# Performance work log

Measured on AMD Instinct MI355X. Metric: run time of the kernel, lower is better.

## Reference

```python
import jax, jax.numpy as jnp
import numpy as np
import math

B, S, H, NH = 2, 2048, 1024, 16
HD = H // NH


def setup_inputs() -> dict:
    key = jax.random.key(0)
    k1, k2, k3 = jax.random.split(key, 3)
    hidden_states = jax.random.normal(k1, (B, S, H), dtype=jnp.float32)
    attention_mask = jnp.zeros((B, 1, 1, S), dtype=jnp.float32)
    w_qkv = jax.random.normal(k2, (3 * H, H), dtype=jnp.float32) * (1.0 / math.sqrt(H))
    w_out = jax.random.normal(k3, (H, H), dtype=jnp.float32) * (1.0 / math.sqrt(H))
    gate = jnp.ones((NH,), dtype=jnp.float32)
    return {"hidden_states": hidden_states, "attention_mask": attention_mask,
            "w_qkv": w_qkv, "w_out": w_out, "gate": gate}


def reference(hidden_states, attention_mask, w_qkv, w_out, gate):
    b, s, h = hidden_states.shape
    nh, hd = NH, HD
    # fused QKV projection (no bias)
    qkv = hidden_states @ w_qkv.T                      # [b, s, 3h]
    qkv = qkv.reshape(b, s, 3, nh, hd)
    q, k, v = jnp.moveaxis(qkv, 2, 0)                  # each [b, s, nh, hd]
    q = q.transpose(0, 2, 1, 3)                        # [b, nh, s, hd]
    k = k.transpose(0, 2, 1, 3)
    v = v.transpose(0, 2, 1, 3)
    scores = jnp.einsum('bhqd,bhkd->bhqk', q, k) / math.sqrt(hd)
    scores = scores + attention_mask                   # broadcast [b,1,1,s]
    probs = jax.nn.softmax(scores, axis=-1)            # dropout p=0 -> identity
    ctx = jnp.einsum('bhqk,bhkd->bhqd', probs, v)      # [b, nh, s, hd]
    ctx = ctx.transpose(0, 2, 1, 3)                    # [b, s, nh, hd]
    ctx = ctx * gate[None, None, :, None]              # per-head gating
    ctx = ctx.reshape(b, s, h)
    out = ctx @ w_out.T
    # all gates active (> 1e-4) -> active_gates/num_heads == 1, no rescale
    return out
```

## Files before the change

kernel.cpp:

```cpp
#include <hip/hip_runtime.h>
#include <stdint.h>


typedef __attribute__((ext_vector_type(8))) short short8;
typedef __attribute__((ext_vector_type(4))) float floatx4;
typedef __attribute__((ext_vector_type(4))) unsigned int uint4v;
typedef __attribute__((ext_vector_type(2))) unsigned int uint2v;

__device__ __forceinline__ unsigned short f2bf(float f) {
    unsigned int u = __float_as_uint(f);
    unsigned int r = u + 0x7fffu + ((u >> 16) & 1u);
    return (unsigned short)(r >> 16);
}
#if __has_builtin(__builtin_amdgcn_cvt_pk_bf16_f32)
__device__ __forceinline__ unsigned int pack_bf2(float lo, float hi) {
    auto v = __builtin_amdgcn_cvt_pk_bf16_f32(lo, hi);
    return __builtin_bit_cast(unsigned int, v);
}
#else
__device__ __forceinline__ unsigned int pack_bf2(float lo, float hi) {
    unsigned int a = __float_as_uint(lo) + 0x8000u;
    unsigned int b = __float_as_uint(hi) + 0x8000u;
    return __builtin_amdgcn_perm(b, a, 0x07060302u);
}
#endif

#if __has_builtin(__builtin_amdgcn_exp2f)
#define EXP2(x) __builtin_amdgcn_exp2f(x)
#else
#define EXP2(x) exp2f(x)
#endif

__device__ __forceinline__ void gl2lds16(const void* g, void* l) {
    __builtin_amdgcn_global_load_lds(
        (const __attribute__((address_space(1))) unsigned int*)g,
        (__attribute__((address_space(3))) unsigned int*)l, 16, 0, 0);
}

#define MFMA32(a, b, c) __builtin_amdgcn_mfma_f32_16x16x32_bf16((a), (b), (c), 0, 0, 0)

__global__ __launch_bounds__(256)
void cvt_all(const float* __restrict__ a, const float* __restrict__ b,
             const float* __restrict__ c, const float* __restrict__ mask,
             unsigned short* __restrict__ oa, unsigned short* __restrict__ ob,
             unsigned short* __restrict__ oc, float* __restrict__ m2b)
{
    int i = blockIdx.x * 256 + threadIdx.x;
    if (i >= 2097152) {
        int off = i - 2097152;
        float4 v = *(const float4*)(mask + (size_t)off * 4);
        const float L2E = 1.44269504f, C2 = -14.4269504f;
        float4 w;
        w.x = fmaf(v.x, L2E, C2); w.y = fmaf(v.y, L2E, C2);
        w.z = fmaf(v.z, L2E, C2); w.w = fmaf(v.w, L2E, C2);
        *(float4*)(m2b + (size_t)off * 4) = w;
        return;
    }
    const float* src; unsigned short* dst; int off;
    if (i < 1048576)      { src = a; dst = oa; off = i; }
    else if (i < 1835008) { src = b; dst = ob; off = i - 1048576; }
    else                  { src = c; dst = oc; off = i - 1835008; }
    float4 v = *(const float4*)(src + (size_t)off * 4);
    uint2v w;
    w[0] = pack_bf2(v.x, v.y);
    w[1] = pack_bf2(v.z, v.w);
    *(uint2v*)(dst + (size_t)off * 4) = w;
}

template<int MODE, int BN>
__global__ __launch_bounds__(256)
void gemm_nt(const unsigned short* __restrict__ A,
             const unsigned short* __restrict__ Bm,
             unsigned short* __restrict__ out0,
             unsigned short* __restrict__ out1,
             unsigned short* __restrict__ out2,
             float* __restrict__ outf,
             int N)
{
    constexpr int BUF = 16384 + BN * 128;
    __shared__ unsigned char smem[2 * BUF];
    const int K = 1024;
    const int NSTEP = 16;
    const int BSL = BN / 32;
    const int tid  = threadIdx.x;
    const int wave = tid >> 6, lane = tid & 63;
    const int l15  = lane & 15, quad = lane >> 4;
    const int wm = wave >> 1, wn = wave & 1;

    int Lid = blockIdx.y * gridDim.x + blockIdx.x;
    int bm = (Lid & 7) * 4 + ((Lid >> 3) & 3);
    int bn = Lid >> 5;

    floatx4 acc[4][BSL];
#pragma unroll
    for (int i = 0; i < 4; i++)
#pragma unroll
        for (int j = 0; j < BSL; j++)
            acc[i][j] = floatx4{0.f, 0.f, 0.f, 0.f};

    int soffA[4], soffB[BSL];
#pragma unroll
    for (int l = 0; l < 4; l++) {
        int s = (wave * 4 + l) * 64 + lane;
        int row = s >> 3;
        soffA[l] = row * K + (((s & 7) ^ (row & 7)) * 8);
    }
#pragma unroll
    for (int l = 0; l < BSL; l++) {
        int s = (wave * BSL + l) * 64 + lane;
        int row = s >> 3;
        soffB[l] = row * K + (((s & 7) ^ (row & 7)) * 8);
    }

    const unsigned short* Abase = A  + (size_t)(bm * 128) * K;
    const unsigned short* Bbase = Bm + (size_t)(bn * BN) * K;

#pragma unroll
    for (int l = 0; l < 4; l++)
        gl2lds16(Abase + (size_t)soffA[l], &smem[(wave * 4 + l) * 1024]);
#pragma unroll
    for (int l = 0; l < BSL; l++)
        gl2lds16(Bbase + (size_t)soffB[l], &smem[16384 + (wave * BSL + l) * 1024]);

    for (int t = 0; t < NSTEP; t++) {
        const int cb = (t & 1) * BUF;
        const int nb = ((t + 1) & 1) * BUF;
        asm volatile("" ::: "memory");
        __builtin_amdgcn_s_barrier();
        asm volatile("" ::: "memory");
        if (t + 1 < NSTEP) {
            const int k0 = (t + 1) * 64;
#pragma unroll
            for (int l = 0; l < 4; l++)
                gl2lds16(Abase + (size_t)soffA[l] + k0, &smem[nb + (wave * 4 + l) * 1024]);
#pragma unroll
            for (int l = 0; l < BSL; l++)
                gl2lds16(Bbase + (size_t)soffB[l] + k0, &smem[nb + 16384 + (wave * BSL + l) * 1024]);
            if (BN == 128) asm volatile("s_waitcnt vmcnt(8)" ::: "memory");
            else           asm volatile("s_waitcnt vmcnt(6)" ::: "memory");
        } else {
            asm volatile("s_waitcnt vmcnt(0)" ::: "memory");
        }
        __builtin_amdgcn_s_barrier();
        asm volatile("" ::: "memory");

#pragma unroll
        for (int s2 = 0; s2 < 2; s2++) {
            short8 af[4], bfr[BSL];
            int c = s2 * 4 + quad;
#pragma unroll
            for (int i = 0; i < 4; i++) {
                int row = wm * 64 + i * 16 + l15;
                af[i] = *(const short8*)(&smem[cb + row * 128 + ((c ^ (row & 7)) * 16)]);
            }
#pragma unroll
            for (int j = 0; j < BSL; j++) {
                int row = wn * (BN / 2) + j * 16 + l15;
                bfr[j] = *(const short8*)(&smem[cb + 16384 + row * 128 + ((c ^ (row & 7)) * 16)]);
            }
#pragma unroll
            for (int i = 0; i < 4; i++)
#pragma unroll
                for (int j = 0; j < BSL; j++)
                    acc[i][j] = MFMA32(af[i], bfr[j], acc[i][j]);
        }
    }

#pragma unroll
    for (int i = 0; i < 4; i++) {
#pragma unroll
        for (int j = 0; j < BSL; j++) {
            int n = bn * BN + wn * (BN / 2) + j * 16 + l15;
#pragma unroll
            for (int r = 0; r < 4; r++) {
                int m = bm * 128 + wm * 64 + i * 16 + quad * 4 + r;
                float fv = acc[i][j][r];
                if (MODE == 1) {
                    outf[(size_t)m * N + n] = fv;
                } else {
                    int t = n >> 10;
                    int h = (n >> 6) & 15;
                    int d = n & 63;
                    int b = m >> 11, si = m & 2047;
                    if (t == 2) {
                        int sip = (si & ~31) | (((si >> 2) & 3) << 3)
                                | (((si >> 4) & 1) << 2) | (si & 3);
                        out2[(((size_t)(b * 16 + h)) * 64 + d) * 2048 + sip] = f2bf(fv);
                    } else {
                        if (t == 0) fv *= 0.18033688f;
                        size_t off = (((size_t)(b * 16 + h)) * 2048 + si) * 64 + d;
                        unsigned short* dst = (t == 0) ? out0 : out1;
                        dst[off] = f2bf(fv);
                    }
                }
            }
        }
    }
}

__global__ __launch_bounds__(256, 2)
void attn_kernel(const unsigned short* __restrict__ Qb,
                 const unsigned short* __restrict__ Kb,
                 const unsigned short* __restrict__ VbT,
                 const float* __restrict__ m2b,
                 const float* __restrict__ gateb,
                 unsigned short* __restrict__ ctx)
{
    __shared__ unsigned char smem[65536];
    const int S = 2048;
    const int tid  = threadIdx.x;
    const int wave = tid >> 6, lane = tid & 63;
    const int l15  = lane & 15, quad = lane >> 4;

    int Lid = blockIdx.y * gridDim.x + blockIdx.x;
    int bh = (Lid & 7) * 4 + ((Lid >> 3) & 3);
    int qc = Lid >> 5;
    const int b = bh >> 4, h = bh & 15;
    const int q0 = qc * 64;

    const size_t headoff = (size_t)bh * S * 64;
    const unsigned short* Qh  = Qb  + headoff;
    const unsigned short* Kh  = Kb  + headoff;
    const unsigned short* VhT = VbT + headoff;
    const float* m2p = m2b + (size_t)b * S;

    const int WB = wave * 16384;

    short8 aq[4][2];
#pragma unroll
    for (int sub = 0; sub < 4; sub++)
#pragma unroll
        for (int s2 = 0; s2 < 2; s2++)
            aq[sub][s2] = *(const short8*)(Qh + (size_t)(q0 + sub * 16 + l15) * 64 + s2 * 32 + quad * 8);

    floatx4 o[4][4];
    floatx4 lq[4];
#pragma unroll
    for (int sub = 0; sub < 4; sub++) {
        lq[sub] = floatx4{0.f, 0.f, 0.f, 0.f};
#pragma unroll
        for (int dt = 0; dt < 4; dt++) o[sub][dt] = floatx4{0.f, 0.f, 0.f, 0.f};
    }

    int koff[4], voff[4];
#pragma unroll
    for (int l = 0; l < 4; l++) {
        int s = l * 64 + lane;
        int key = s >> 3;
        koff[l] = key * 64 + (((s & 7) ^ (key & 7)) * 8);
        int d = s >> 2;
        voff[l] = d * 2048 + (((s & 3) ^ (d & 3)) * 8);
    }
    int qkoff[2];
#pragma unroll
    for (int s2 = 0; s2 < 2; s2++)
        qkoff[s2] = l15 * 128 + (((s2 * 4 + quad) ^ (l15 & 7)) * 16);
    const int pvoff = 4096 + l15 * 64 + ((quad ^ (l15 & 3)) * 16);

    const uint4v onesu = {0x3F803F80u, 0x3F803F80u, 0x3F803F80u, 0x3F803F80u};
    const short8 ONES = __builtin_bit_cast(short8, onesu);

    {
        const unsigned short* kg = Kh + (size_t)(wave * 32) * 64;
        const unsigned short* vg = VhT + wave * 32;
#pragma unroll
        for (int l = 0; l < 4; l++) {
            gl2lds16(kg + koff[l], &smem[WB + l * 1024]);
            gl2lds16(vg + voff[l], &smem[WB + 4096 + l * 1024]);
        }
    }

    for (int i = 0; i < 16; i++) {
        const int kb = (wave + 4 * i) * 32;
        floatx4 mf[2];
#pragma unroll
        for (int t = 0; t < 2; t++)
            mf[t] = *(const floatx4*)(m2p + kb + t * 16 + quad * 4);
        asm volatile("" ::: "memory");
        {
            const int kbn = (wave + 4 * ((i + 1) & 15)) * 32;
            const int hb = WB + ((i + 1) & 1) * 8192;
            const unsigned short* kg = Kh + (size_t)kbn * 64;
            const unsigned short* vg = VhT + kbn;
#pragma unroll
            for (int l = 0; l < 4; l++) {
                gl2lds16(kg + koff[l], &smem[hb + l * 1024]);
                gl2lds16(vg + voff[l], &smem[hb + 4096 + l * 1024]);
            }
        }
        asm volatile("s_waitcnt vmcnt(8)" ::: "memory");

        const int cb = WB + (i & 1) * 8192;
        short8 vf[4];
#pragma unroll
        for (int dt = 0; dt < 4; dt++)
            vf[dt] = *(const short8*)(&smem[cb + pvoff + dt * 1024]);
        short8 kf[2][2];
#pragma unroll
        for (int t = 0; t < 2; t++)
#pragma unroll
            for (int s2 = 0; s2 < 2; s2++)
                kf[t][s2] = *(const short8*)(&smem[cb + qkoff[s2] + t * 2048]);

#pragma unroll
        for (int sub = 0; sub < 4; sub++) {
            floatx4 st0 = MFMA32(kf[0][0], aq[sub][0], mf[0]);
            floatx4 st1 = MFMA32(kf[1][0], aq[sub][0], mf[1]);
            st0 = MFMA32(kf[0][1], aq[sub][1], st0);
            st1 = MFMA32(kf[1][1], aq[sub][1], st1);
            float e00 = EXP2(st0[0]), e01 = EXP2(st0[1]);
            float e02 = EXP2(st0[2]), e03 = EXP2(st0[3]);
            float e10 = EXP2(st1[0]), e11 = EXP2(st1[1]);
            float e12 = EXP2(st1[2]), e13 = EXP2(st1[3]);
            uint4v pu = {pack_bf2(e00, e01), pack_bf2(e02, e03),
                         pack_bf2(e10, e11), pack_bf2(e12, e13)};
            short8 pf = __builtin_bit_cast(short8, pu);
#pragma unroll
            for (int dt = 0; dt < 4; dt++)
                o[sub][dt] = MFMA32(vf[dt], pf, o[sub][dt]);
            lq[sub] = MFMA32(ONES, pf, lq[sub]);
        }
    }

    asm volatile("s_waitcnt vmcnt(0)" ::: "memory");

    floatx4 ro[4];
#pragma unroll
    for (int ph = 0; ph < 2; ph++) {
        __syncthreads();
#pragma unroll
        for (int sub = 0; sub < 4; sub++)
#pragma unroll
            for (int d2 = 0; d2 < 2; d2++)
                *(floatx4*)(&smem[(((wave * 4 + sub) * 2 + d2) * 64 + lane) * 16]) = o[sub][ph * 2 + d2];
        __syncthreads();
#pragma unroll
        for (int d2 = 0; d2 < 2; d2++) {
            floatx4 acc = floatx4{0.f, 0.f, 0.f, 0.f};
#pragma unroll
            for (int w2 = 0; w2 < 4; w2++)
                acc += *(const floatx4*)(&smem[(((w2 * 4 + wave) * 2 + d2) * 64 + lane) * 16]);
            ro[ph * 2 + d2] = acc;
        }
    }
    __syncthreads();
#pragma unroll
    for (int sub = 0; sub < 4; sub++)
        *(floatx4*)(&smem[((wave * 4 + sub) * 64 + lane) * 16]) = lq[sub];
    __syncthreads();
    floatx4 rl = floatx4{0.f, 0.f, 0.f, 0.f};
#pragma unroll
    for (int w2 = 0; w2 < 4; w2++)
        rl += *(const floatx4*)(&smem[((w2 * 4 + wave) * 64 + lane) * 16]);

    float iv = gateb[h] / rl[0];
    size_t base = ((size_t)(b * 2048 + q0 + wave * 16 + l15)) * 1024 + h * 64 + quad * 4;
#pragma unroll
    for (int dt = 0; dt < 4; dt++) {
        uint2v w;
        w[0] = pack_bf2(ro[dt][0] * iv, ro[dt][1] * iv);
        w[1] = pack_bf2(ro[dt][2] * iv, ro[dt][3] * iv);
        *(uint2v*)(ctx + base + dt * 16) = w;
    }
}

extern "C" void kernel_launch(void* const* d_in, const int* in_sizes, int n_in,
                              void* d_out, int out_size, void* d_ws, size_t ws_size,
                              hipStream_t stream)
{
    const float* hidden = (const float*)d_in[0];
    const float* mask   = (const float*)d_in[1];
    const float* w_qkv  = (const float*)d_in[2];
    const float* w_out  = (const float*)d_in[3];
    const float* gate   = (const float*)d_in[4];
    float* out = (float*)d_out;

    unsigned short* q_buf = (unsigned short*)d_ws;
    unsigned short* k_buf = q_buf + 4194304;
    unsigned short* v_buf = k_buf + 4194304;
    unsigned short* c_buf = v_buf + 4194304;
    unsigned short* h_bf  = c_buf + 4194304;
    unsigned short* wq_bf = h_bf  + 4194304;
    unsigned short* wo_bf = wq_bf + 3145728;
    float* m2_buf = (float*)(wo_bf + 1048576);

    cvt_all<<<8196, 256, 0, stream>>>(hidden, w_qkv, w_out, mask,
                                      h_bf, wq_bf, wo_bf, m2_buf);

    gemm_nt<0, 128><<<dim3(24, 32), 256, 0, stream>>>(h_bf, wq_bf, q_buf, k_buf, v_buf, nullptr, 3072);
    attn_kernel<<<dim3(32, 32), 256, 0, stream>>>(q_buf, k_buf, v_buf, m2_buf, gate, c_buf);
    gemm_nt<1, 64><<<dim3(16, 32), 256, 0, stream>>>(c_buf, wo_bf, nullptr, nullptr, nullptr, out, 1024);
}
```

Baseline: 186.6 us.

## Load K/V fragments directly from global memory, drop LDS double buffering

The attention kernel no longer stages K and V tiles through shared memory with async global-to-LDS copies and double buffering. Each lane now reads its K and V MFMA fragments straight from global memory (relying on cache). Shared memory shrinks to 32KB, used only for the final cross-wave reduction, and launch bounds rise to 4 blocks per CU to gain occupancy. This trades explicit prefetch and latency hiding for more resident waves and less LDS traffic. Global loads become less coalesced and their latency is exposed within each iteration.

```diff
diff --git a/kernel.cpp b/kernel.cpp
--- a/kernel.cpp
+++ b/kernel.cpp
@@ -198,7 +198,7 @@
     }
 }
 
-__global__ __launch_bounds__(256, 2)
+__global__ __launch_bounds__(256, 4)
 void attn_kernel(const unsigned short* __restrict__ Qb,
                  const unsigned short* __restrict__ Kb,
                  const unsigned short* __restrict__ VbT,
@@ -206,7 +206,7 @@
                  const float* __restrict__ gateb,
                  unsigned short* __restrict__ ctx)
 {
-    __shared__ unsigned char smem[65536];
+    __shared__ unsigned char smem[32768];
     const int S = 2048;
     const int tid  = threadIdx.x;
     const int wave = tid >> 6, lane = tid & 63;
@@ -224,7 +224,8 @@
     const unsigned short* VhT = VbT + headoff;
     const float* m2p = m2b + (size_t)b * S;
 
-    const int WB = wave * 16384;
+    const unsigned short* kp = Kh  + (size_t)l15 * 64   + quad * 8;
+    const unsigned short* vp = VhT + (size_t)l15 * 2048 + quad * 8;
 
     short8 aq[4][2];
 #pragma unroll
@@ -242,65 +243,25 @@
         for (int dt = 0; dt < 4; dt++) o[sub][dt] = floatx4{0.f, 0.f, 0.f, 0.f};
     }
 
-    int koff[4], voff[4];
-#pragma unroll
-    for (int l = 0; l < 4; l++) {
-        int s = l * 64 + lane;
-        int key = s >> 3;
-        koff[l] = key * 64 + (((s & 7) ^ (key & 7)) * 8);
-        int d = s >> 2;
-        voff[l] = d * 2048 + (((s & 3) ^ (d & 3)) * 8);
-    }
-    int qkoff[2];
-#pragma unroll
-    for (int s2 = 0; s2 < 2; s2++)
-        qkoff[s2] = l15 * 128 + (((s2 * 4 + quad) ^ (l15 & 7)) * 16);
-    const int pvoff = 4096 + l15 * 64 + ((quad ^ (l15 & 3)) * 16);
-
     const uint4v onesu = {0x3F803F80u, 0x3F803F80u, 0x3F803F80u, 0x3F803F80u};
     const short8 ONES = __builtin_bit_cast(short8, onesu);
 
-    {
-        const unsigned short* kg = Kh + (size_t)(wave * 32) * 64;
-        const unsigned short* vg = VhT + wave * 32;
-#pragma unroll
-        for (int l = 0; l < 4; l++) {
-            gl2lds16(kg + koff[l], &smem[WB + l * 1024]);
-            gl2lds16(vg + voff[l], &smem[WB + 4096 + l * 1024]);
-        }
-    }
-
     for (int i = 0; i < 16; i++) {
         const int kb = (wave + 4 * i) * 32;
+        short8 kf[2][2];
+#pragma unroll
+        for (int t = 0; t < 2; t++)
+#pragma unroll
+            for (int s2 = 0; s2 < 2; s2++)
+                kf[t][s2] = *(const short8*)(kp + (size_t)kb * 64 + t * 1024 + s2 * 32);
         floatx4 mf[2];
 #pragma unroll
         for (int t = 0; t < 2; t++)
             mf[t] = *(const floatx4*)(m2p + kb + t * 16 + quad * 4);
-        asm volatile("" ::: "memory");
-        {
-            const int kbn = (wave + 4 * ((i + 1) & 15)) * 32;
-            const int hb = WB + ((i + 1) & 1) * 8192;
-            const unsigned short* kg = Kh + (size_t)kbn * 64;
-            const unsigned short* vg = VhT + kbn;
-#pragma unroll
-            for (int l = 0; l < 4; l++) {
-                gl2lds16(kg + koff[l], &smem[hb + l * 1024]);
-                gl2lds16(vg + voff[l], &smem[hb + 4096 + l * 1024]);
-            }
-        }
-        asm volatile("s_waitcnt vmcnt(8)" ::: "memory");
-
-        const int cb = WB + (i & 1) * 8192;
         short8 vf[4];
 #pragma unroll
         for (int dt = 0; dt < 4; dt++)
-            vf[dt] = *(const short8*)(&smem[cb + pvoff + dt * 1024]);
-        short8 kf[2][2];
-#pragma unroll
-        for (int t = 0; t < 2; t++)
-#pragma unroll
-            for (int s2 = 0; s2 < 2; s2++)
-                kf[t][s2] = *(const short8*)(&smem[cb + qkoff[s2] + t * 2048]);
+            vf[dt] = *(const short8*)(vp + (size_t)dt * 32768 + kb);
 
 #pragma unroll
         for (int sub = 0; sub < 4; sub++) {
@@ -322,8 +283,6 @@
         }
     }
 
-    asm volatile("s_waitcnt vmcnt(0)" ::: "memory");
-
     floatx4 ro[4];
 #pragma unroll
     for (int ph = 0; ph < 2; ph++) {
```

Result: slower. 377.7 us (+102.4%).
